# Kernel tuning notes

Measured on AMD Instinct MI355X. Metric: run time of the kernel, lower is better.

## Reference

```python
import jax, jax.numpy as jnp
import numpy as np

N_E = 8192
E_DIM = 256
BETA = 0.25
DECAY = 0.99
EPSILON = 1e-05


def setup_inputs() -> dict:
    key = jax.random.key(0)
    k1, k2 = jax.random.split(key)
    z = jax.random.normal(k1, (16, 2048, E_DIM), dtype=jnp.float32)
    # xavier_uniform for [n_e, e_dim]
    bound = float(np.sqrt(6.0 / (N_E + E_DIM)))
    embeddings = jax.random.uniform(k2, (N_E, E_DIM), dtype=jnp.float32,
                                    minval=-bound, maxval=bound)
    return {"z": z, "embeddings": embeddings}


def reference(z, embeddings):
    old_shape = z.shape
    z_flat = z.reshape(-1, E_DIM)  # [N, D]

    # squared-distance: ||z||^2 + ||e||^2 - 2 z.e  -> [N, n_e]
    distances = (jnp.sum(z_flat * z_flat, axis=1, keepdims=True)
                 + jnp.sum(embeddings * embeddings, axis=1)
                 - 2.0 * jnp.einsum('nd,kd->nk', z_flat, embeddings))
    idx = jnp.argmin(distances, axis=1)  # [N] int

    z_q = embeddings[idx].reshape(old_shape)

    # --- EMA codebook update (training, first step: counter 0 -> 1,
    # hidden starts at 0 so the bias-corrected average equals the value) ---
    ones = jnp.ones_like(idx, dtype=jnp.float32)
    bins = jax.ops.segment_sum(ones, idx, num_segments=N_E)          # [n_e]
    dw = jax.ops.segment_sum(z_flat, idx, num_segments=N_E)          # [n_e, D]
    ema_cluster = bins   # EMA step 1 with zero-init hidden == value
    ema_dw = dw
    n = jnp.sum(ema_cluster)
    cluster = (ema_cluster + EPSILON) / (n + N_E * EPSILON) * n
    new_embeddings = ema_dw / cluster[:, None]

    loss = BETA * jnp.mean((z - jax.lax.stop_gradient(z_q)) ** 2)
    z_q_st = z + jax.lax.stop_gradient(z_q - z)  # straight-through
    return z_q_st, idx, loss, new_embeddings
```

## Files before the change

### kernel.cpp

```cpp
#include <hip/hip_runtime.h>
#include <math.h>
#include <float.h>

#define N_ROWS 32768
#define EDIM 256
#define NE 8192
#define NTILES 64
#define DELTA 1.6e-3f
#define RB 8

typedef unsigned int uint32;
typedef unsigned long long uint64;
typedef __attribute__((ext_vector_type(8))) _Float16 f16x8;
typedef __attribute__((ext_vector_type(4))) float f32x4;

#define OFF_ZCAT    ((size_t)0)
#define OFF_ECAT    ((size_t)33554432)
#define OFF_ET      ((size_t)37748736)
#define OFF_EN      ((size_t)46268416)
#define OFF_PV      ((size_t)46301184)
#define OFF_PI      ((size_t)54689792)
#define OFF_PV2     ((size_t)63078400)
#define OFF_IDX     ((size_t)71467008)
#define OFF_BINS    ((size_t)71598080)
#define OFF_PACKED  ((size_t)71630848)
#define OFF_FLAGCNT ((size_t)71892992)
#define OFF_FLAGGED ((size_t)71893504)

__device__ __forceinline__ uint32 pack2_f16(float a, float b) {
    _Float16 ha = (_Float16)a;
    _Float16 hb = (_Float16)b;
    unsigned short ua = __builtin_bit_cast(unsigned short, ha);
    unsigned short ub = __builtin_bit_cast(unsigned short, hb);
    return (uint32)ua | ((uint32)ub << 16);
}

__device__ __forceinline__ void gload_lds16(const void* g, void* l) {
    __builtin_amdgcn_global_load_lds(
        (const __attribute__((address_space(1))) uint32*)g,
        (__attribute__((address_space(3))) uint32*)l, 16, 0, 0);
}

__device__ __forceinline__ float np_pairwise_sumsq(const float* a) {
#pragma clang fp contract(off)
    float h0, h1;
    #pragma unroll 1
    for (int hb = 0; hb < 2; ++hb) {
        const float* p = a + hb * 128;
        float r0=p[0]*p[0], r1=p[1]*p[1], r2=p[2]*p[2], r3=p[3]*p[3],
              r4=p[4]*p[4], r5=p[5]*p[5], r6=p[6]*p[6], r7=p[7]*p[7];
        #pragma unroll 1
        for (int i = 8; i < 128; i += 8) {
            r0 += p[i+0]*p[i+0]; r1 += p[i+1]*p[i+1];
            r2 += p[i+2]*p[i+2]; r3 += p[i+3]*p[i+3];
            r4 += p[i+4]*p[i+4]; r5 += p[i+5]*p[i+5];
            r6 += p[i+6]*p[i+6]; r7 += p[i+7]*p[i+7];
        }
        float s = ((r0+r1)+(r2+r3))+((r4+r5)+(r6+r7));
        if (hb == 0) h0 = s; else h1 = s;
    }
    return h0 + h1;
}

__global__ void k_prep(const float* __restrict__ Z, const float* __restrict__ E,
                       unsigned short* __restrict__ Zcat, unsigned short* __restrict__ Ecat,
                       float* __restrict__ ET, float* __restrict__ en,
                       uint64* __restrict__ packed, int* __restrict__ hist,
                       int* __restrict__ flagcnt) {
    int b = blockIdx.x;
    int t = threadIdx.x;
    if (b < 4096) {
        int r = b * 8 + (t >> 5);
        int u = t & 31;
        int c = u >> 2, q = u & 3;
        int lq = q ^ ((r >> 1) & 3);
        int k0 = c * 32 + lq * 8;
        const float4* zp = (const float4*)(Z + (size_t)r * EDIM + k0);
        float4 a = zp[0], bb = zp[1];
        float f[8] = {a.x,a.y,a.z,a.w,bb.x,bb.y,bb.z,bb.w};
        uint32 o[4];
        #pragma unroll
        for (int j = 0; j < 4; ++j) o[j] = pack2_f16(f[2*j], f[2*j+1]);
        *(uint4*)(Zcat + (size_t)r * 256 + c * 32 + q * 8) = make_uint4(o[0],o[1],o[2],o[3]);
    } else if (b < 5120) {
        int r = (b - 4096) * 8 + (t >> 5);
        int u = t & 31;
        int c = u >> 2, q = u & 3;
        int lq = q ^ ((r >> 1) & 3);
        int k0 = c * 32 + lq * 8;
        const float4* ep = (const float4*)(E + (size_t)r * EDIM + k0);
        float4 a = ep[0], bb = ep[1];
        float f[8] = {a.x,a.y,a.z,a.w,bb.x,bb.y,bb.z,bb.w};
        uint32 o[4];
        #pragma unroll
        for (int j = 0; j < 4; ++j) o[j] = pack2_f16(256.0f*f[2*j], 256.0f*f[2*j+1]);
        *(uint4*)(Ecat + (size_t)r * 256 + c * 32 + q * 8) = make_uint4(o[0],o[1],o[2],o[3]);
        #pragma unroll
        for (int j = 0; j < 8; ++j) ET[(size_t)(k0 + j) * NE + r] = f[j];
    } else if (b < 5152) {
        int k = (b - 5120) * 256 + t;
        en[k] = np_pairwise_sumsq(E + (size_t)k * EDIM);
    } else if (b < 5184) {
        int i = (b - 5152) * 256 + t;
        #pragma unroll
        for (int j = 0; j < 4; ++j) packed[i + j*8192] = 0xFFFFFFFFFFFFFFFFull;
    } else {
        hist[(b - 5184) * 256 + t] = 0;
        if (b == 5184 && t == 0) *flagcnt = 0;
    }
}

__device__ __forceinline__ uint32 float_key(float v) {
    uint32 b = __float_as_uint(v);
    return (b & 0x80000000u) ? ~b : (b | 0x80000000u);
}

__global__ __launch_bounds__(256, 4) void k_gemm(
    const unsigned short* __restrict__ Zcat, const unsigned short* __restrict__ Ecat,
    const float* __restrict__ enorm,
    float* __restrict__ pv, int* __restrict__ pi, float* __restrict__ pv2)
{
    __shared__ __align__(16) char UB[33024];
    __shared__ float ens[128];
    __shared__ float fv1[128]; __shared__ int fi1[128]; __shared__ float fv2[128];

    unsigned short* As0 = (unsigned short*)(UB);
    unsigned short* As1 = (unsigned short*)(UB + 8192);
    unsigned short* Bs0 = (unsigned short*)(UB + 16384);
    unsigned short* Bs1 = (unsigned short*)(UB + 24576);

    int t = threadIdx.x;
    int nt = blockIdx.x & 63, mt = blockIdx.x >> 6;
    int wid = t >> 6, lane = t & 63;
    int wmg = wid >> 1, wng = wid & 1;
    int wm = wmg * 64, wn = wng * 64;

    if (t < 128) ens[t] = enorm[nt*128 + t];

    int j0 = wid*2, j1 = j0 + 1;
    int r0 = j0*16 + (lane >> 2), r1 = j1*16 + (lane >> 2);
    int c8 = (lane & 3) * 8;
    const unsigned short* gA0 = Zcat + (size_t)(mt*128 + r0)*256 + c8;
    const unsigned short* gA1 = Zcat + (size_t)(mt*128 + r1)*256 + c8;
    const unsigned short* gB0 = Ecat + (size_t)(nt*128 + r0)*256 + c8;
    const unsigned short* gB1 = Ecat + (size_t)(nt*128 + r1)*256 + c8;
    unsigned short* lA0s0 = As0 + j0*512;  unsigned short* lA1s0 = As0 + j1*512;
    unsigned short* lA0s1 = As1 + j0*512;  unsigned short* lA1s1 = As1 + j1*512;
    unsigned short* lB0s0 = Bs0 + j0*512;  unsigned short* lB1s0 = Bs0 + j1*512;
    unsigned short* lB0s1 = Bs1 + j0*512;  unsigned short* lB1s1 = Bs1 + j1*512;

    f32x4 acc[4][4];
    #pragma unroll
    for (int i = 0; i < 4; ++i)
        #pragma unroll
        for (int j = 0; j < 4; ++j) acc[i][j] = (f32x4){0.f,0.f,0.f,0.f};

    int frow = lane & 15, q = lane >> 4;
    int sw = (frow >> 1) & 3;
    const unsigned short* a0Base = As0 + (wm + frow)*32 + ((q ^ sw) * 8);
    const unsigned short* a1Base = As1 + (wm + frow)*32 + ((q ^ sw) * 8);
    const unsigned short* b0Base = Bs0 + (wn + frow)*32 + ((q ^ sw) * 8);
    const unsigned short* b1Base = Bs1 + (wn + frow)*32 + ((q ^ sw) * 8);

    #pragma unroll 1
    for (int it = 0; it < 4; ++it) {
        int aOff = it * 64;
        gload_lds16(gA0 + aOff,      lA0s0);
        gload_lds16(gA1 + aOff,      lA1s0);
        gload_lds16(gA0 + aOff + 32, lA0s1);
        gload_lds16(gA1 + aOff + 32, lA1s1);
        gload_lds16(gB0 + aOff,      lB0s0);
        gload_lds16(gB1 + aOff,      lB1s0);
        gload_lds16(gB0 + aOff + 32, lB0s1);
        gload_lds16(gB1 + aOff + 32, lB1s1);
        __syncthreads();
        f16x8 af[4], bfr[4];
        #pragma unroll
        for (int i = 0; i < 4; ++i) bfr[i] = *(const f16x8*)(b0Base + i*16*32);
        #pragma unroll
        for (int i = 0; i < 4; ++i) af[i] = *(const f16x8*)(a0Base + i*16*32);
        #pragma unroll
        for (int i = 0; i < 4; ++i)
            #pragma unroll
            for (int j = 0; j < 4; ++j)
                acc[i][j] = __builtin_amdgcn_mfma_f32_16x16x32_f16(af[i], bfr[j], acc[i][j], 0, 0, 0);
        #pragma unroll
        for (int i = 0; i < 4; ++i) bfr[i] = *(const f16x8*)(b1Base + i*16*32);
        #pragma unroll
        for (int i = 0; i < 4; ++i) af[i] = *(const f16x8*)(a1Base + i*16*32);
        #pragma unroll
        for (int i = 0; i < 4; ++i)
            #pragma unroll
            for (int j = 0; j < 4; ++j)
                acc[i][j] = __builtin_amdgcn_mfma_f32_16x16x32_f16(af[i], bfr[j], acc[i][j], 0, 0, 0);
        __syncthreads();
    }

    float ensr[4]; int nn[4];
    #pragma unroll
    for (int j = 0; j < 4; ++j) {
        int nl = wn + j*16 + frow;
        nn[j] = nt*128 + nl;
        ensr[j] = ens[nl];
    }
    uint4* P = (uint4*)UB;
    int gbase = wng*64 + wmg*32 + q*4;

    #pragma unroll
    for (int ih = 0; ih < 2; ++ih) {
        #pragma unroll
        for (int i2 = 0; i2 < 2; ++i2) {
            int i = ih*2 + i2;
            #pragma unroll
            for (int r = 0; r < 4; ++r) {
                float s0 = fmaf(-0.0078125f, acc[i][0][r], ensr[0]);
                float s1 = fmaf(-0.0078125f, acc[i][1][r], ensr[1]);
                float s2 = fmaf(-0.0078125f, acc[i][2][r], ensr[2]);
                float s3 = fmaf(-0.0078125f, acc[i][3][r], ensr[3]);
                float v1 = s0; int i1 = nn[0];
                float v2 = fmaxf(v1, s1);
                if (s1 < v1) i1 = nn[1];
                v1 = fminf(v1, s1);
                v2 = fminf(v2, fmaxf(v1, s2));
                if (s2 < v1) i1 = nn[2];
                v1 = fminf(v1, s2);
                v2 = fminf(v2, fmaxf(v1, s3));
                if (s3 < v1) i1 = nn[3];
                v1 = fminf(v1, s3);
                P[frow*129 + gbase + i2*16 + r] =
                    make_uint4(__float_as_uint(v1), (uint32)i1, __float_as_uint(v2), 0u);
            }
        }
        __syncthreads();
        if (t < 128) {
            const uint4* base = P + t;
            uint4 e0 = base[0];
            float v1 = __uint_as_float(e0.x); int i1 = (int)e0.y;
            float v2 = __uint_as_float(e0.z);
            #pragma unroll
            for (int f = 1; f < 16; ++f) {
                uint4 e = base[f*129];
                float ov1 = __uint_as_float(e.x), ov2 = __uint_as_float(e.z);
                v2 = fminf(fminf(v2, ov2), fmaxf(v1, ov1));
                if (ov1 < v1) i1 = (int)e.y;
                v1 = fminf(v1, ov1);
            }
            fv1[t] = v1; fi1[t] = i1; fv2[t] = v2;
        }
        __syncthreads();
        if (t < 64) {
            float v1 = fv1[t], v2 = fv2[t]; int i1 = fi1[t];
            float ov1 = fv1[64+t], ov2 = fv2[64+t];
            v2 = fminf(fminf(v2, ov2), fmaxf(v1, ov1));
            if (ov1 < v1) i1 = fi1[64+t];
            v1 = fminf(v1, ov1);
            size_t o = (size_t)nt * N_ROWS + mt*128 + (t>>5)*64 + ih*32 + (t&31);
            pv[o] = v1; pi[o] = i1; pv2[o] = v2;
        }
    }
}

__global__ void k_merge(const float* __restrict__ pv, const int* __restrict__ pi,
                        const float* __restrict__ pv2,
                        float* __restrict__ out_idx_f, int* __restrict__ idxint,
                        int* __restrict__ flagcnt, int* __restrict__ flagged) {
    int g = blockIdx.x * 256 + threadIdx.x;
    float B1 = FLT_MAX, B2 = FLT_MAX; int I1 = 0;
    #pragma unroll 1
    for (int p = 0; p < NTILES; ++p) {
        size_t o = (size_t)p * N_ROWS + g;
        float v1 = pv[o], v2 = pv2[o]; int i1 = pi[o];
        if (v1 < B1) { B2 = fminf(B1, v2); B1 = v1; I1 = i1; }
        else B2 = fminf(B2, v1);
    }
    out_idx_f[g] = (float)I1;
    idxint[g] = I1;
    if (B2 - B1 < DELTA) {
        int slot = atomicAdd(flagcnt, 1);
        flagged[slot] = g;
    }
}

__global__ void k_phaseB(const float* __restrict__ Z, const float* __restrict__ ET,
                         const float* __restrict__ enorm,
                         const int* __restrict__ flagcnt, const int* __restrict__ flagged,
                         uint64* __restrict__ packed) {
    __shared__ float zl[RB][256];
    __shared__ float znl[RB];
    __shared__ int rows[RB];
    __shared__ float sv[256]; __shared__ int si[256];
    int t = threadIdx.x;
    int cnt = *flagcnt; if (cnt > N_ROWS) cnt = N_ROWS;
    int ngrp = (cnt + RB - 1) / RB;
    int ntask = ngrp * 8;
    #pragma unroll 1
    for (int task = blockIdx.x; task < ntask; task += gridDim.x) {
        int slice = task & 7;
        int g0 = (task >> 3) * RB;
        __syncthreads();
        if (t < RB) {
            int f = g0 + t;
            rows[t] = flagged[f < cnt ? f : g0];
        }
        __syncthreads();
        #pragma unroll
        for (int rr = 0; rr < RB; ++rr) zl[rr][t] = Z[(size_t)rows[rr]*EDIM + t];
        __syncthreads();
        if (t < RB) znl[t] = np_pairwise_sumsq(&zl[t][0]);
        __syncthreads();

        float acc[RB][4];
        #pragma unroll
        for (int rr = 0; rr < RB; ++rr)
            #pragma unroll
            for (int c = 0; c < 4; ++c) acc[rr][c] = 0.f;
        const float* eb = ET + slice*1024 + t;
        #pragma unroll 1
        for (int d = 0; d < 256; ++d) {
            const float* ep = eb + (size_t)d * NE;
            float v0 = ep[0], v1 = ep[256], v2 = ep[512], v3 = ep[768];
            #pragma unroll
            for (int rr = 0; rr < RB; ++rr) {
                float zd = zl[rr][d];
                acc[rr][0] = fmaf(zd, v0, acc[rr][0]);
                acc[rr][1] = fmaf(zd, v1, acc[rr][1]);
                acc[rr][2] = fmaf(zd, v2, acc[rr][2]);
                acc[rr][3] = fmaf(zd, v3, acc[rr][3]);
            }
        }
        #pragma unroll 1
        for (int rr = 0; rr < RB; ++rr) {
            int row = rows[rr];
            float zn = znl[rr];
            float bv = FLT_MAX; int bi = 0x7fffffff;
            {
#pragma clang fp contract(off)
                #pragma unroll
                for (int c = 0; c < 4; ++c) {
                    int k = slice*1024 + c*256 + t;
                    float S  = zn + enorm[k];
                    float tw = 2.0f * acc[rr][c];
                    float sc = S - tw;
                    if (sc < bv || (sc == bv && k < bi)) { bv = sc; bi = k; }
                }
            }
            sv[t] = bv; si[t] = bi;
            __syncthreads();
            for (int st = 128; st > 0; st >>= 1) {
                if (t < st) {
                    float ov = sv[t+st]; int oi = si[t+st];
                    if (ov < sv[t] || (ov == sv[t] && oi < si[t])) { sv[t] = ov; si[t] = oi; }
                }
                __syncthreads();
            }
            if (t == 0) {
                uint64 pk = ((uint64)float_key(sv[0]) << 32) | (uint32)si[0];
                atomicMin(packed + row, pk);
            }
            __syncthreads();
        }
    }
}

__global__ void k_taila(const float* __restrict__ Z, const float* __restrict__ E,
                        int* __restrict__ idxint, const uint64* __restrict__ packed,
                        float* __restrict__ out0, float* __restrict__ out_idx_f,
                        int* __restrict__ hist, float* __restrict__ lossp) {
    __shared__ float wsum[4];
    int t = threadIdx.x;
    int w = t >> 6, lane = t & 63;
    int row = blockIdx.x * 4 + w;
    int idx = idxint[row];
    uint64 pk = packed[row];
    if (pk != 0xFFFFFFFFFFFFFFFFull) {
        idx = (int)(uint32)(pk & 0xffffffffu);
        if (lane == 0) { out_idx_f[row] = (float)idx; idxint[row] = idx; }
    }
    float4 z4 = ((const float4*)Z)[(size_t)row * 64 + lane];
    float4 e4 = ((const float4*)E)[(size_t)idx * 64 + lane];
    float4 d4; d4.x = e4.x - z4.x; d4.y = e4.y - z4.y; d4.z = e4.z - z4.z; d4.w = e4.w - z4.w;
    float4 o;  o.x = z4.x + d4.x;  o.y = z4.y + d4.y;  o.z = z4.z + d4.z;  o.w = z4.w + d4.w;
    ((float4*)out0)[(size_t)row * 64 + lane] = o;
    float q2 = d4.x*d4.x + d4.y*d4.y + d4.z*d4.z + d4.w*d4.w;
    #pragma unroll
    for (int off = 32; off > 0; off >>= 1) q2 += __shfl_down(q2, off, 64);
    if (lane == 0) { wsum[w] = q2; atomicAdd(&hist[idx], 1); }
    __syncthreads();
    if (t == 0) lossp[blockIdx.x] = wsum[0] + wsum[1] + wsum[2] + wsum[3];
}

__global__ void k_scan(const int* __restrict__ hist,
                       int* __restrict__ cursor, int* __restrict__ offs) {
    __shared__ int part[256];
    int t = threadIdx.x;
    int loc[32];
    int s = 0;
    #pragma unroll
    for (int j = 0; j < 32; ++j) { loc[j] = s; s += hist[t*32 + j]; }
    part[t] = s;
    __syncthreads();
    #pragma unroll
    for (int off = 1; off < 256; off <<= 1) {
        int u = (t >= off) ? part[t - off] : 0;
        __syncthreads();
        part[t] += u;
        __syncthreads();
    }
    int base = part[t] - s;
    #pragma unroll
    for (int j = 0; j < 32; ++j) {
        int o = base + loc[j];
        offs[t*32 + j] = o;
        cursor[t*32 + j] = o;
    }
}

__global__ void k_tailb(const int* __restrict__ idxint,
                        int* __restrict__ cursor, int* __restrict__ rowlist) {
    int g = blockIdx.x * 256 + threadIdx.x;
    int idx = idxint[g];
    int pos = atomicAdd(&cursor[idx], 1);
    rowlist[pos] = g;
}

__global__ void k_dw(const float* __restrict__ Z, const int* __restrict__ hist,
                     const int* __restrict__ offs, const int* __restrict__ rowlist,
                     const float* __restrict__ lossp,
                     float* __restrict__ out3, float* __restrict__ out2) {
    __shared__ double red[256];
    int k = blockIdx.x;
    int t = threadIdx.x;
    int cnt = hist[k];
    int start = offs[k];
    float s0 = 0.f, s1 = 0.f;
    int j = 0;
    #pragma unroll 1
    for (; j + 1 < cnt; j += 2) {
        int ra = rowlist[start + j];
        int rb = rowlist[start + j + 1];
        s0 += Z[(size_t)ra * EDIM + t];
        s1 += Z[(size_t)rb * EDIM + t];
    }
    if (j < cnt) s0 += Z[(size_t)rowlist[start + j] * EDIM + t];
    float sum = s0 + s1;
    float cl = ((float)cnt + 1e-5f) / (32768.0f + 8192.0f * 1e-5f) * 32768.0f;
    out3[(size_t)k * EDIM + t] = sum / cl;
    if (k == 0) {
        double s = 0.0;
        #pragma unroll 1
        for (int p = t; p < 8192; p += 256) s += (double)lossp[p];
        red[t] = s;
        __syncthreads();
        #pragma unroll
        for (int st = 128; st > 0; st >>= 1) {
            if (t < st) red[t] += red[t + st];
            __syncthreads();
        }
        if (t == 0) out2[0] = 0.25f * (float)(red[0] / 8388608.0);
    }
}

extern "C" void kernel_launch(void* const* d_in, const int* in_sizes, int n_in,
                              void* d_out, int out_size, void* d_ws, size_t ws_size,
                              hipStream_t stream) {
    const float* Z = (const float*)d_in[0];
    const float* E = (const float*)d_in[1];
    float* out  = (float*)d_out;
    float* out0 = out;
    float* out1 = out + 8388608;
    float* out2 = out1 + 32768;
    float* out3 = out2 + 1;

    char* ws = (char*)d_ws;
    unsigned short* Zcat = (unsigned short*)(ws + OFF_ZCAT);
    unsigned short* Ecat = (unsigned short*)(ws + OFF_ECAT);
    float*  ET      = (float*)(ws + OFF_ET);
    float*  enorm   = (float*)(ws + OFF_EN);
    float*  pv      = (float*)(ws + OFF_PV);
    int*    pi      = (int*)  (ws + OFF_PI);
    float*  pv2     = (float*)(ws + OFF_PV2);
    int*    idxint  = (int*)  (ws + OFF_IDX);
    int*    hist    = (int*)  (ws + OFF_BINS);
    uint64* packed  = (uint64*)(ws + OFF_PACKED);
    int*    flagcnt = (int*)  (ws + OFF_FLAGCNT);
    int*    flagged = (int*)  (ws + OFF_FLAGGED);
    float*  lossp   = (float*)(ws + OFF_PV);
    int*    rowlist = (int*)  (ws + OFF_PV + 32768);
    int*    cursor  = (int*)  (ws + OFF_PV2);
    int*    offs    = (int*)  (ws + OFF_PV2 + 32768);

    k_prep   <<<5216,         256, 0, stream>>>(Z, E, Zcat, Ecat, ET, enorm,
                                                packed, hist, flagcnt);
    k_gemm   <<<256 * NTILES, 256, 0, stream>>>(Zcat, Ecat, enorm, pv, pi, pv2);
    k_merge  <<<N_ROWS / 256, 256, 0, stream>>>(pv, pi, pv2, out1, idxint, flagcnt, flagged);
    k_phaseB <<<2048,         256, 0, stream>>>(Z, ET, enorm, flagcnt, flagged, packed);
    k_taila  <<<N_ROWS / 4,   256, 0, stream>>>(Z, E, idxint, packed, out0, out1, hist, lossp);
    k_scan   <<<1,            256, 0, stream>>>(hist, cursor, offs);
    k_tailb  <<<N_ROWS / 256, 256, 0, stream>>>(idxint, cursor, rowlist);
    k_dw     <<<NE,           256, 0, stream>>>(Z, hist, offs, rowlist, lossp, out3, out2);
}
```

Before: 429.9 us.

## Double-buffer GEMM k-loop loads and transpose codebook through LDS

The distance GEMM main loop now prefetches the next 32-wide k-chunk into the alternate LDS buffer while computing on the current one. The goal is to overlap global-to-LDS loads with MFMA work instead of loading both halves and then computing. Separately, the codebook transpose in the prep kernel now stages an 8-row tile in shared memory and writes ET with coalesced float4 stores, replacing strided scalar stores. The diff context does not show how the pipelined loop synchronises between the prefetch into one buffer and the reads of the other, so there is a risk of LDS races.

```diff
diff --git a/kernel.cpp b/kernel.cpp
--- a/kernel.cpp
+++ b/kernel.cpp
@@ -67,6 +67,7 @@
                        float* __restrict__ ET, float* __restrict__ en,
                        uint64* __restrict__ packed, int* __restrict__ hist,
                        int* __restrict__ flagcnt) {
+    __shared__ float tile[8][264];
     int b = blockIdx.x;
     int t = threadIdx.x;
     if (b < 4096) {
@@ -83,7 +84,9 @@
         for (int j = 0; j < 4; ++j) o[j] = pack2_f16(f[2*j], f[2*j+1]);
         *(uint4*)(Zcat + (size_t)r * 256 + c * 32 + q * 8) = make_uint4(o[0],o[1],o[2],o[3]);
     } else if (b < 5120) {
-        int r = (b - 4096) * 8 + (t >> 5);
+        int eb = b - 4096;
+        int r8 = t >> 5;
+        int r = eb * 8 + r8;
         int u = t & 31;
         int c = u >> 2, q = u & 3;
         int lq = q ^ ((r >> 1) & 3);
@@ -95,8 +98,15 @@
         #pragma unroll
         for (int j = 0; j < 4; ++j) o[j] = pack2_f16(256.0f*f[2*j], 256.0f*f[2*j+1]);
         *(uint4*)(Ecat + (size_t)r * 256 + c * 32 + q * 8) = make_uint4(o[0],o[1],o[2],o[3]);
-        #pragma unroll
-        for (int j = 0; j < 8; ++j) ET[(size_t)(k0 + j) * NE + r] = f[j];
+        *(float4*)&tile[r8][k0]     = make_float4(f[0], f[1], f[2], f[3]);
+        *(float4*)&tile[r8][k0 + 4] = make_float4(f[4], f[5], f[6], f[7]);
+        __syncthreads();
+        float4 lo, hi;
+        lo.x = tile[0][t]; lo.y = tile[1][t]; lo.z = tile[2][t]; lo.w = tile[3][t];
+        hi.x = tile[4][t]; hi.y = tile[5][t]; hi.z = tile[6][t]; hi.w = tile[7][t];
+        float* dst = ET + (size_t)t * NE + eb * 8;
+        *(float4*)dst = lo;
+        *(float4*)(dst + 4) = hi;
     } else if (b < 5152) {
         int k = (b - 5120) * 256 + t;
         en[k] = np_pairwise_sumsq(E + (size_t)k * EDIM);
@@ -162,32 +172,36 @@
     const unsigned short* b0Base = Bs0 + (wn + frow)*32 + ((q ^ sw) * 8);
     const unsigned short* b1Base = Bs1 + (wn + frow)*32 + ((q ^ sw) * 8);
 
+    gload_lds16(gA0, lA0s0);
+    gload_lds16(gA1, lA1s0);
+    gload_lds16(gB0, lB0s0);
+    gload_lds16(gB1, lB1s0);
+    __syncthreads();
+
     #pragma unroll 1
-    for (int it = 0; it < 4; ++it) {
-        int aOff = it * 64;
-        gload_lds16(gA0 + aOff,      lA0s0);
-        gload_lds16(gA1 + aOff,      lA1s0);
-        gload_lds16(gA0 + aOff + 32, lA0s1);
-        gload_lds16(gA1 + aOff + 32, lA1s1);
-        gload_lds16(gB0 + aOff,      lB0s0);
-        gload_lds16(gB1 + aOff,      lB1s0);
-        gload_lds16(gB0 + aOff + 32, lB0s1);
-        gload_lds16(gB1 + aOff + 32, lB1s1);
-        __syncthreads();
+    for (int c = 0; c < 8; ++c) {
+        int nxt = c + 1;
+        if (nxt < 8) {
+            int aOff = nxt * 32;
+            if (nxt & 1) {
+                gload_lds16(gA0 + aOff, lA0s1);
+                gload_lds16(gA1 + aOff, lA1s1);
+                gload_lds16(gB0 + aOff, lB0s1);
+                gload_lds16(gB1 + aOff, lB1s1);
+            } else {
+                gload_lds16(gA0 + aOff, lA0s0);
+                gload_lds16(gA1 + aOff, lA1s0);
+                gload_lds16(gB0 + aOff, lB0s0);
+                gload_lds16(gB1 + aOff, lB1s0);
+            }
+        }
+        const unsigned short* aB = (c & 1) ? a1Base : a0Base;
+        const unsigned short* bB = (c & 1) ? b1Base : b0Base;
         f16x8 af[4], bfr[4];
         #pragma unroll
-        for (int i = 0; i < 4; ++i) bfr[i] = *(const f16x8*)(b0Base + i*16*32);
-        #pragma unroll
-        for (int i = 0; i < 4; ++i) af[i] = *(const f16x8*)(a0Base + i*16*32);
-        #pragma unroll
-        for (int i = 0; i < 4; ++i)
-            #pragma unroll
-            for (int j = 0; j < 4; ++j)
-                acc[i][j] = __builtin_amdgcn_mfma_f32_16x16x32_f16(af[i], bfr[j], acc[i][j], 0, 0, 0);
-        #pragma unroll
-        for (int i = 0; i < 4; ++i) bfr[i] = *(const f16x8*)(b1Base + i*16*32);
-        #pragma unroll
-        for (int i = 0; i < 4; ++i) af[i] = *(const f16x8*)(a1Base + i*16*32);
+        for (int i = 0; i < 4; ++i) bfr[i] = *(const f16x8*)(bB + i*16*32);
+        #pragma unroll
+        for (int i = 0; i < 4; ++i) af[i] = *(const f16x8*)(aB + i*16*32);
         #pragma unroll
         for (int i = 0; i < 4; ++i)
             #pragma unroll
```

Result: no change. 436.6 us (+1.6%).
